# Kernel optimization log

Measured on AMD Instinct MI355X. Metric: run time of the kernel, lower is better.

Reference implementation:

```python
import jax, jax.numpy as jnp
import numpy as np

EMBED = 1024
HEADS = 16
HEAD_DIM = EMBED // HEADS


def setup_inputs() -> dict:
    key = jax.random.key(0)
    k1, k2, k3 = jax.random.split(key, 3)
    hidden_states = jax.random.normal(k1, (2, 2048, EMBED), dtype=jnp.float32)
    # Conv1D weights are stored (nx, nf): y = x @ W + b
    c_attn_w = jax.random.normal(k2, (EMBED, 3 * EMBED), dtype=jnp.float32) * 0.02
    c_attn_b = jnp.zeros((3 * EMBED,), dtype=jnp.float32)
    c_proj_w = jax.random.normal(k3, (EMBED, EMBED), dtype=jnp.float32) * 0.02
    c_proj_b = jnp.zeros((EMBED,), dtype=jnp.float32)
    return {
        "hidden_states": hidden_states,
        "c_attn_w": c_attn_w,
        "c_attn_b": c_attn_b,
        "c_proj_w": c_proj_w,
        "c_proj_b": c_proj_b,
    }


def reference(hidden_states, c_attn_w, c_attn_b, c_proj_w, c_proj_b):
    B, S, E = hidden_states.shape
    H, D = HEADS, HEAD_DIM
    fused = hidden_states @ c_attn_w + c_attn_b  # [B,S,3E]
    q, k, v = jnp.split(fused, 3, axis=-1)
    # split heads -> [B,H,S,D]
    q = q.reshape(B, S, H, D).transpose(0, 2, 1, 3)
    k = k.reshape(B, S, H, D).transpose(0, 2, 1, 3)
    v = v.reshape(B, S, H, D).transpose(0, 2, 1, 3)
    scores = jnp.einsum("bhqd,bhkd->bhqk", q, k) / jnp.sqrt(jnp.float32(D))
    probs = jax.nn.softmax(scores, axis=-1)  # NOTE: no causal mask in source
    attn = jnp.einsum("bhqk,bhkd->bhqd", probs, v)
    out = attn.transpose(0, 2, 1, 3).reshape(B, S, E)
    return out @ c_proj_w + c_proj_b
```

## Files before the change

kernel.cpp:

```cpp
#include <hip/hip_runtime.h>
#include <hip/hip_bf16.h>
#include <cstdint>
#include <cstddef>

#define E_ 1024
#define H_ 16
#define D_ 64
#define B_ 2
#define S_ 2048
#define T_ 4096
#define NQ_ 3072

typedef __bf16 bf16_t;
typedef bf16_t bf16x8 __attribute__((ext_vector_type(8)));
typedef float f32x4 __attribute__((ext_vector_type(4)));

static __device__ __forceinline__ unsigned short f2bf(float f) {
    __hip_bfloat16 h = __float2bfloat16(f);
    return __builtin_bit_cast(unsigned short, h);
}
static __device__ __forceinline__ unsigned pack2(float a, float b) {
    return (unsigned)f2bf(a) | ((unsigned)f2bf(b) << 16);
}
static __device__ __forceinline__ bf16x8 ld_frag(const unsigned short* p) {
    uint4 u = *reinterpret_cast<const uint4*>(p);
    return __builtin_bit_cast(bf16x8, u);
}
static __device__ __forceinline__ void cp16(unsigned short* lds, const unsigned short* g) {
    __builtin_amdgcn_global_load_lds(
        (const __attribute__((address_space(1))) unsigned int*)g,
        (__attribute__((address_space(3))) unsigned int*)lds, 16, 0, 0);
}
static __device__ __forceinline__ f32x4 mfma16(bf16x8 a, bf16x8 b, f32x4 c) {
    return __builtin_amdgcn_mfma_f32_16x16x32_bf16(a, b, c, 0, 0, 0);
}

__global__ __launch_bounds__(256) void k_cvt(const float* __restrict__ in,
                                             unsigned short* __restrict__ out, int n) {
    int i = (blockIdx.x * 256 + threadIdx.x) * 4;
    if (i < n) {
        float4 v = *reinterpret_cast<const float4*>(in + i);
        uint2 o;
        o.x = pack2(v.x, v.y);
        o.y = pack2(v.z, v.w);
        *reinterpret_cast<uint2*>(out + i) = o;
    }
}

__global__ __launch_bounds__(256) void k_wt(const float* __restrict__ in,
                                            unsigned short* __restrict__ out, int K, int N) {
    __shared__ float t[32][33];
    int n0 = blockIdx.x * 32, k0 = blockIdx.y * 32;
    int tx = threadIdx.x, ty = threadIdx.y;
    for (int j = 0; j < 4; j++) {
        int r = ty + j * 8;
        t[r][tx] = in[(size_t)(k0 + r) * N + n0 + tx];
    }
    __syncthreads();
    for (int j = 0; j < 4; j++) {
        int r = ty + j * 8;
        out[(size_t)(n0 + r) * K + k0 + tx] = f2bf(t[tx][r]);
    }
}

static __device__ __forceinline__ void gemm_tile_128(
    const unsigned short* __restrict__ A,
    const unsigned short* __restrict__ Bt,
    int Ktot, int m0, int n0,
    unsigned short* As, unsigned short* Bs,
    f32x4 acc[4][4])
{
    const int t = threadIdx.x;
    const int w = t >> 6, lane = t & 63, lr = lane & 15, lq = lane >> 4;
    const int wm = (w >> 1) * 64, wn = (w & 1) * 64;
    for (int mt = 0; mt < 4; mt++)
        for (int nt = 0; nt < 4; nt++)
            acc[mt][nt] = (f32x4){0.f, 0.f, 0.f, 0.f};

    for (int kt = 0; kt < Ktot; kt += 32) {
        __syncthreads();
        for (int i = 0; i < 2; i++) {
            int c = t + i * 256;
            int row = c >> 2, kp = (c & 3) * 8;
            cp16(&As[c * 8], &A[(size_t)(m0 + row) * Ktot + kt + kp]);
        }
        for (int i = 0; i < 2; i++) {
            int c = t + i * 256;
            int row = c >> 2, kp = (c & 3) * 8;
            cp16(&Bs[c * 8], &Bt[(size_t)(n0 + row) * Ktot + kt + kp]);
        }
        __syncthreads();
        bf16x8 af[4], bfr[4];
        for (int mt = 0; mt < 4; mt++) af[mt]  = ld_frag(&As[(wm + mt * 16 + lr) * 32 + lq * 8]);
        for (int nt = 0; nt < 4; nt++) bfr[nt] = ld_frag(&Bs[(wn + nt * 16 + lr) * 32 + lq * 8]);
        for (int mt = 0; mt < 4; mt++)
            for (int nt = 0; nt < 4; nt++)
                acc[mt][nt] = mfma16(af[mt], bfr[nt], acc[mt][nt]);
    }
}

__global__ __launch_bounds__(256) void k_qkv(
    const unsigned short* __restrict__ Ab, const unsigned short* __restrict__ Wt,
    const float* __restrict__ bias,
    unsigned short* __restrict__ Qb, unsigned short* __restrict__ Kb,
    unsigned short* __restrict__ Vb)
{
    __shared__ __attribute__((aligned(16))) unsigned short As[128 * 32];
    __shared__ __attribute__((aligned(16))) unsigned short Bs[128 * 32];
    f32x4 acc[4][4];
    int m0 = blockIdx.x * 128, n0 = blockIdx.y * 128;
    gemm_tile_128(Ab, Wt, E_, m0, n0, As, Bs, acc);

    int t = threadIdx.x, w = t >> 6, lane = t & 63, lr = lane & 15, lq = lane >> 4;
    int wm = (w >> 1) * 64, wn = (w & 1) * 64;
    int sector = (n0 >> 10);
    for (int nt = 0; nt < 4; nt++) {
        int n = n0 + wn + nt * 16 + lr;
        float bv = bias[n];
        int nn = n & 1023, h = nn >> 6, d = nn & 63;
        for (int mt = 0; mt < 4; mt++) {
            for (int i = 0; i < 4; i++) {
                int tok = m0 + wm + mt * 16 + lq * 4 + i;
                int b = tok >> 11, s = tok & 2047;
                float v = acc[mt][nt][i] + bv;
                if (sector == 0) {
                    Qb[(((size_t)(b * H_ + h) * S_ + s) << 6) + d] = f2bf(v * 0.18033688f);
                } else if (sector == 1) {
                    Kb[(((size_t)(b * H_ + h) * S_ + s) << 6) + d] = f2bf(v);
                } else {
                    Vb[(((size_t)(b * H_ + h) * D_ + d) << 11) + s] = f2bf(v);
                }
            }
        }
    }
}

__global__ __launch_bounds__(256) void k_attn(
    const unsigned short* __restrict__ Qb, const unsigned short* __restrict__ Kb,
    const unsigned short* __restrict__ Vb, unsigned short* __restrict__ Ob)
{
    __shared__ __attribute__((aligned(16))) unsigned short Ks[2][64 * 64];
    __shared__ __attribute__((aligned(16))) unsigned short Vt[2][64 * 64];
    __shared__ __attribute__((aligned(16))) unsigned short Ps[4][16 * 64];

    const int t = threadIdx.x, w = t >> 6, lane = t & 63, lr = lane & 15, lq = lane >> 4;
    const int h = blockIdx.y, b = blockIdx.z;
    const size_t head = ((size_t)(b * H_ + h)) * (S_ * D_);
    const unsigned short* Qh = Qb + head;
    const unsigned short* Kh = Kb + head;
    const unsigned short* Vh = Vb + head;
    const int q0 = blockIdx.x * 64 + w * 16;
    const int swz = lr & 7;

    bf16x8 qa[2];
    for (int kk = 0; kk < 2; kk++)
        qa[kk] = ld_frag(&Qh[(size_t)(q0 + lr) * 64 + kk * 32 + lq * 8]);

    f32x4 o[4];
    for (int i = 0; i < 4; i++) o[i] = (f32x4){0.f, 0.f, 0.f, 0.f};
    float lsum = 0.f;
    unsigned short* Pw = Ps[w];

    auto stage = [&](int bb, int kt) {
        for (int i = 0; i < 2; i++) {
            int c = t + i * 256;
            int row = c >> 3, sp = c & 7, seg = sp ^ (row & 7);
            cp16(&Ks[bb][c * 8], &Kh[(size_t)(kt + row) * 64 + seg * 8]);
        }
        for (int i = 0; i < 2; i++) {
            int c = t + i * 256;
            int d = c >> 3, sp = c & 7, seg = sp ^ (d & 7);
            cp16(&Vt[bb][c * 8], &Vh[(size_t)d * S_ + kt + seg * 8]);
        }
    };

    stage(0, 0);
    asm volatile("s_waitcnt vmcnt(0)" ::: "memory");
    __syncthreads();

    int cur = 0;
    for (int kt = 0; kt < S_; kt += 64) {
        if (kt + 64 < S_) stage(cur ^ 1, kt + 64);

        const unsigned short* Kc = Ks[cur];
        const unsigned short* Vc = Vt[cur];

        float pexp[4][4];
        for (int tau = 0; tau < 4; tau++) {
            f32x4 z = (f32x4){0.f, 0.f, 0.f, 0.f};
            bf16x8 kf0 = ld_frag(&Kc[(tau * 16 + lr) * 64 + ((0 + lq) ^ swz) * 8]);
            bf16x8 kf1 = ld_frag(&Kc[(tau * 16 + lr) * 64 + ((4 + lq) ^ swz) * 8]);
            __builtin_amdgcn_s_setprio(1);
            z = mfma16(kf0, qa[0], z);
            z = mfma16(kf1, qa[1], z);
            __builtin_amdgcn_s_setprio(0);
            for (int r = 0; r < 4; r++) {
                float p = __builtin_amdgcn_exp2f(z[r]);
                pexp[tau][r] = p;
                lsum += p;
            }
        }
        for (int tau = 0; tau < 4; tau++) {
            uint2 pk;
            pk.x = pack2(pexp[tau][0], pexp[tau][1]);
            pk.y = pack2(pexp[tau][2], pexp[tau][3]);
            int seg = (tau * 2 + (lq >> 1)) ^ swz;
            *reinterpret_cast<uint2*>(&Pw[lr * 64 + seg * 8 + (lq & 1) * 4]) = pk;
        }
        for (int kk = 0; kk < 2; kk++) {
            bf16x8 pf = ld_frag(&Pw[lr * 64 + ((kk * 4 + lq) ^ swz) * 8]);
            __builtin_amdgcn_s_setprio(1);
            for (int t2 = 0; t2 < 4; t2++) {
                bf16x8 vf = ld_frag(&Vc[(t2 * 16 + lr) * 64 + ((kk * 4 + lq) ^ swz) * 8]);
                o[t2] = mfma16(vf, pf, o[t2]);
            }
            __builtin_amdgcn_s_setprio(0);
        }

        asm volatile("s_waitcnt vmcnt(0)" ::: "memory");
        __syncthreads();
        cur ^= 1;
    }

    lsum += __shfl_xor(lsum, 16, 64);
    lsum += __shfl_xor(lsum, 32, 64);
    float inv = 1.0f / lsum;

    int s = q0 + lr;
    size_t rowoff = ((size_t)(b * S_ + s)) * E_ + h * 64;
    for (int t2 = 0; t2 < 4; t2++) {
        uint2 pk;
        pk.x = pack2(o[t2][0] * inv, o[t2][1] * inv);
        pk.y = pack2(o[t2][2] * inv, o[t2][3] * inv);
        *reinterpret_cast<uint2*>(&Ob[rowoff + t2 * 16 + lq * 4]) = pk;
    }
}

__global__ __launch_bounds__(256) void k_proj(
    const unsigned short* __restrict__ Ab, const unsigned short* __restrict__ Wt,
    const float* __restrict__ bias, float* __restrict__ out)
{
    __shared__ __attribute__((aligned(16))) unsigned short As[128 * 32];
    __shared__ __attribute__((aligned(16))) unsigned short Bs[128 * 32];
    f32x4 acc[4][4];
    int m0 = blockIdx.x * 128, n0 = blockIdx.y * 128;
    gemm_tile_128(Ab, Wt, E_, m0, n0, As, Bs, acc);

    int t = threadIdx.x, w = t >> 6, lane = t & 63, lr = lane & 15, lq = lane >> 4;
    int wm = (w >> 1) * 64, wn = (w & 1) * 64;
    for (int nt = 0; nt < 4; nt++) {
        int n = n0 + wn + nt * 16 + lr;
        float bv = bias[n];
        for (int mt = 0; mt < 4; mt++)
            for (int i = 0; i < 4; i++) {
                int tok = m0 + wm + mt * 16 + lq * 4 + i;
                out[(size_t)tok * E_ + n] = acc[mt][nt][i] + bv;
            }
    }
}

extern "C" void kernel_launch(void* const* d_in, const int* in_sizes, int n_in,
                              void* d_out, int out_size, void* d_ws, size_t ws_size,
                              hipStream_t stream) {
    const float* hs = (const float*)d_in[0];
    const float* w1 = (const float*)d_in[1];
    const float* b1 = (const float*)d_in[2];
    const float* w2 = (const float*)d_in[3];
    const float* b2 = (const float*)d_in[4];
    float* out = (float*)d_out;

    char* ws = (char*)d_ws;
    unsigned short* hb  = (unsigned short*)(ws);
    unsigned short* w1t = (unsigned short*)(ws + (size_t)( 8 << 20));
    unsigned short* w2t = (unsigned short*)(ws + (size_t)(14 << 20));
    unsigned short* Qb  = (unsigned short*)(ws + (size_t)(16 << 20));
    unsigned short* Kb  = (unsigned short*)(ws + (size_t)(24 << 20));
    unsigned short* Vb  = (unsigned short*)(ws + (size_t)(32 << 20));
    unsigned short* Ao  = (unsigned short*)(ws + (size_t)(40 << 20));

    k_cvt<<<dim3(T_ * E_ / 1024), dim3(256), 0, stream>>>(hs, hb, T_ * E_);
    k_wt<<<dim3(NQ_ / 32, E_ / 32), dim3(32, 8), 0, stream>>>(w1, w1t, E_, NQ_);
    k_wt<<<dim3(E_ / 32, E_ / 32), dim3(32, 8), 0, stream>>>(w2, w2t, E_, E_);
    k_qkv<<<dim3(T_ / 128, NQ_ / 128), dim3(256), 0, stream>>>(hb, w1t, b1, Qb, Kb, Vb);
    k_attn<<<dim3(S_ / 64, H_, B_), dim3(256), 0, stream>>>(Qb, Kb, Vb, Ao);
    k_proj<<<dim3(T_ / 128, E_ / 128), dim3(256), 0, stream>>>(Ao, w2t, b2, out);
}
```

Baseline: 203.6 us.

## Process two query tiles per warp in attention to reuse K/V fragments

Each attention block now covers 128 queries instead of 64, with every warp holding two 16-row query tiles. Each K fragment and V fragment read from LDS feeds two MFMAs, which halves LDS and global K/V traffic per query. The P-tile writes are fused into the exp loop, bf16 packing uses the v_cvt_pk_bf16_f32 instruction, and the key loop is unrolled by 2. In exchange the grid has half as many blocks (512), register pressure rises, and the P scratch space in LDS doubles.

```diff
diff --git a/kernel.cpp b/kernel.cpp
--- a/kernel.cpp
+++ b/kernel.cpp
@@ -21,6 +21,11 @@
 }
 static __device__ __forceinline__ unsigned pack2(float a, float b) {
     return (unsigned)f2bf(a) | ((unsigned)f2bf(b) << 16);
+}
+static __device__ __forceinline__ unsigned cvt_pk(float a, float b) {
+    unsigned r;
+    asm("v_cvt_pk_bf16_f32 %0, %1, %2" : "=v"(r) : "v"(a), "v"(b));
+    return r;
 }
 static __device__ __forceinline__ bf16x8 ld_frag(const unsigned short* p) {
     uint4 u = *reinterpret_cast<const uint4*>(p);
@@ -141,7 +146,7 @@
 {
     __shared__ __attribute__((aligned(16))) unsigned short Ks[2][64 * 64];
     __shared__ __attribute__((aligned(16))) unsigned short Vt[2][64 * 64];
-    __shared__ __attribute__((aligned(16))) unsigned short Ps[4][16 * 64];
+    __shared__ __attribute__((aligned(16))) unsigned short Ps[4][32 * 64];
 
     const int t = threadIdx.x, w = t >> 6, lane = t & 63, lr = lane & 15, lq = lane >> 4;
     const int h = blockIdx.y, b = blockIdx.z;
@@ -149,16 +154,18 @@
     const unsigned short* Qh = Qb + head;
     const unsigned short* Kh = Kb + head;
     const unsigned short* Vh = Vb + head;
-    const int q0 = blockIdx.x * 64 + w * 16;
+    const int q0 = blockIdx.x * 128 + w * 16;
     const int swz = lr & 7;
 
-    bf16x8 qa[2];
-    for (int kk = 0; kk < 2; kk++)
-        qa[kk] = ld_frag(&Qh[(size_t)(q0 + lr) * 64 + kk * 32 + lq * 8]);
-
-    f32x4 o[4];
-    for (int i = 0; i < 4; i++) o[i] = (f32x4){0.f, 0.f, 0.f, 0.f};
-    float lsum = 0.f;
+    bf16x8 qa[2][2];
+    for (int qh = 0; qh < 2; qh++)
+        for (int kk = 0; kk < 2; kk++)
+            qa[qh][kk] = ld_frag(&Qh[(size_t)(q0 + qh * 64 + lr) * 64 + kk * 32 + lq * 8]);
+
+    f32x4 o[2][4];
+    for (int qh = 0; qh < 2; qh++)
+        for (int i = 0; i < 4; i++) o[qh][i] = (f32x4){0.f, 0.f, 0.f, 0.f};
+    float lsum[2] = {0.f, 0.f};
     unsigned short* Pw = Ps[w];
 
     auto stage = [&](int bb, int kt) {
@@ -179,40 +186,42 @@
     __syncthreads();
 
     int cur = 0;
+#pragma unroll 2
     for (int kt = 0; kt < S_; kt += 64) {
         if (kt + 64 < S_) stage(cur ^ 1, kt + 64);
 
         const unsigned short* Kc = Ks[cur];
         const unsigned short* Vc = Vt[cur];
 
-        float pexp[4][4];
         for (int tau = 0; tau < 4; tau++) {
-            f32x4 z = (f32x4){0.f, 0.f, 0.f, 0.f};
             bf16x8 kf0 = ld_frag(&Kc[(tau * 16 + lr) * 64 + ((0 + lq) ^ swz) * 8]);
             bf16x8 kf1 = ld_frag(&Kc[(tau * 16 + lr) * 64 + ((4 + lq) ^ swz) * 8]);
-            __builtin_amdgcn_s_setprio(1);
-            z = mfma16(kf0, qa[0], z);
-            z = mfma16(kf1, qa[1], z);
-            __builtin_amdgcn_s_setprio(0);
-            for (int r = 0; r < 4; r++) {
-                float p = __builtin_amdgcn_exp2f(z[r]);
-                pexp[tau][r] = p;
-                lsum += p;
-            }
-        }
-        for (int tau = 0; tau < 4; tau++) {
-            uint2 pk;
-            pk.x = pack2(pexp[tau][0], pexp[tau][1]);
-            pk.y = pack2(pexp[tau][2], pexp[tau][3]);
-            int seg = (tau * 2 + (lq >> 1)) ^ swz;
-            *reinterpret_cast<uint2*>(&Pw[lr * 64 + seg * 8 + (lq & 1) * 4]) = pk;
+            for (int qh = 0; qh < 2; qh++) {
+                f32x4 z = (f32x4){0.f, 0.f, 0.f, 0.f};
+                __builtin_amdgcn_s_setprio(1);
+                z = mfma16(kf0, qa[qh][0], z);
+                z = mfma16(kf1, qa[qh][1], z);
+                __builtin_amdgcn_s_setprio(0);
+                float e0 = __builtin_amdgcn_exp2f(z[0]);
+                float e1 = __builtin_amdgcn_exp2f(z[1]);
+                float e2 = __builtin_amdgcn_exp2f(z[2]);
+                float e3 = __builtin_amdgcn_exp2f(z[3]);
+                lsum[qh] += (e0 + e1) + (e2 + e3);
+                uint2 pk;
+                pk.x = cvt_pk(e0, e1);
+                pk.y = cvt_pk(e2, e3);
+                int seg = (tau * 2 + (lq >> 1)) ^ swz;
+                *reinterpret_cast<uint2*>(&Pw[(qh * 16 + lr) * 64 + seg * 8 + (lq & 1) * 4]) = pk;
+            }
         }
         for (int kk = 0; kk < 2; kk++) {
-            bf16x8 pf = ld_frag(&Pw[lr * 64 + ((kk * 4 + lq) ^ swz) * 8]);
+            bf16x8 pf0 = ld_frag(&Pw[(lr) * 64 + ((kk * 4 + lq) ^ swz) * 8]);
+            bf16x8 pf1 = ld_frag(&Pw[(16 + lr) * 64 + ((kk * 4 + lq) ^ swz) * 8]);
             __builtin_amdgcn_s_setprio(1);
             for (int t2 = 0; t2 < 4; t2++) {
                 bf16x8 vf = ld_frag(&Vc[(t2 * 16 + lr) * 64 + ((kk * 4 + lq) ^ swz) * 8]);
-                o[t2] = mfma16(vf, pf, o[t2]);
+                o[0][t2] = mfma16(vf, pf0, o[0][t2]);
+                o[1][t2] = mfma16(vf, pf1, o[1][t2]);
             }
             __builtin_amdgcn_s_setprio(0);
         }
@@ -222,17 +231,20 @@
         cur ^= 1;
     }
 
-    lsum += __shfl_xor(lsum, 16, 64);
-    lsum += __shfl_xor(lsum, 32, 64);
-    float inv = 1.0f / lsum;
-
-    int s = q0 + lr;
-    size_t rowoff = ((size_t)(b * S_ + s)) * E_ + h * 64;
-    for (int t2 = 0; t2 < 4; t2++) {
-        uint2 pk;
-        pk.x = pack2(o[t2][0] * inv, o[t2][1] * inv);
-        pk.y = pack2(o[t2][2] * inv, o[t2][3] * inv);
-        *reinterpret_cast<uint2*>(&Ob[rowoff + t2 * 16 + lq * 4]) = pk;
+    for (int qh = 0; qh < 2; qh++) {
+        float ls = lsum[qh];
+        ls += __shfl_xor(ls, 16, 64);
+        ls += __shfl_xor(ls, 32, 64);
+        float inv = 1.0f / ls;
+
+        int s = q0 + qh * 64 + lr;
+        size_t rowoff = ((size_t)(b * S_ + s)) * E_ + h * 64;
+        for (int t2 = 0; t2 < 4; t2++) {
+            uint2 pk;
+            pk.x = cvt_pk(o[qh][t2][0] * inv, o[qh][t2][1] * inv);
+            pk.y = cvt_pk(o[qh][t2][2] * inv, o[qh][t2][3] * inv);
+            *reinterpret_cast<uint2*>(&Ob[rowoff + t2 * 16 + lq * 4]) = pk;
+        }
     }
 }
 
@@ -282,6 +294,6 @@
     k_wt<<<dim3(NQ_ / 32, E_ / 32), dim3(32, 8), 0, stream>>>(w1, w1t, E_, NQ_);
     k_wt<<<dim3(E_ / 32, E_ / 32), dim3(32, 8), 0, stream>>>(w2, w2t, E_, E_);
     k_qkv<<<dim3(T_ / 128, NQ_ / 128), dim3(256), 0, stream>>>(hb, w1t, b1, Qb, Kb, Vb);
-    k_attn<<<dim3(S_ / 64, H_, B_), dim3(256), 0, stream>>>(Qb, Kb, Vb, Ao);
+    k_attn<<<dim3(S_ / 128, H_, B_), dim3(256), 0, stream>>>(Qb, Kb, Vb, Ao);
     k_proj<<<dim3(T_ / 128, E_ / 128), dim3(256), 0, stream>>>(Ao, w2t, b2, out);
 }
```

Measured after the change: 194.3 us. -4.6%, faster.
